# Kernel tuning notes

Measured on AMD Instinct MI355X. Metric: run time of the kernel, lower is better.

The kernel has to match this reference:

```python
import jax, jax.numpy as jnp
import numpy as np

N = 100000      # nodes
E = 1600000     # edges (avg degree 16)
IN_F, HID, OUT_F, NC = 384, 128, 64, 2
EPS = 1e-5
NEG_SLOPE = 0.01


def _layernorm(x, g, b):
    m = jnp.mean(x, axis=-1, keepdims=True)
    v = jnp.var(x, axis=-1, keepdims=True)
    return (x - m) * jax.lax.rsqrt(v + EPS) * g + b


def _graph_conv(x, edge_index, edge_weight, w_rel, b_rel, w_root):
    # PyG GraphConv: lin_rel(scatter_add(w_e * x[src] -> dst)) + lin_root(x)
    src, dst = edge_index[0], edge_index[1]
    msg = x[src] * edge_weight[:, None]                      # [E, C]
    agg = jax.ops.segment_sum(msg, dst, num_segments=x.shape[0])  # [N, C]
    return agg @ w_rel.T + b_rel + x @ w_root.T


def _xavier(key, shape):
    fan_in, fan_out = shape[1], shape[0]
    lim = float(np.sqrt(6.0 / (fan_in + fan_out)))
    return jax.random.uniform(key, shape, jnp.float32, -lim, lim)


def setup_inputs() -> dict:
    key = jax.random.key(0)
    ks = jax.random.split(key, 10)
    x = jax.random.normal(ks[0], (N, IN_F), jnp.float32)
    edge_index = jax.random.randint(ks[1], (2, E), 0, N, jnp.int64)
    edge_attr = jax.random.uniform(ks[2], (E,), jnp.float32)
    return {
        "x": x,
        "edge_index": edge_index,
        "edge_attr": edge_attr,
        "ln1_g": jnp.ones((IN_F,), jnp.float32),
        "ln1_b": jnp.zeros((IN_F,), jnp.float32),
        "fc1_w": _xavier(ks[3], (HID, IN_F)),
        "fc1_b": jnp.zeros((HID,), jnp.float32),
        "c1_wrel": _xavier(ks[4], (HID, HID)),
        "c1_brel": jnp.zeros((HID,), jnp.float32),
        "c1_wroot": _xavier(ks[5], (HID, HID)),
        "c2_wrel": _xavier(ks[6], (OUT_F, HID)),
        "c2_brel": jnp.zeros((OUT_F,), jnp.float32),
        "c2_wroot": _xavier(ks[7], (OUT_F, HID)),
        "ln2_g": jnp.ones((OUT_F,), jnp.float32),
        "ln2_b": jnp.zeros((OUT_F,), jnp.float32),
        "fc2_w": _xavier(ks[8], (NC, OUT_F)),
        "fc2_b": jnp.zeros((NC,), jnp.float32),
    }


def reference(x, edge_index, edge_attr,
              ln1_g, ln1_b, fc1_w, fc1_b,
              c1_wrel, c1_brel, c1_wroot,
              c2_wrel, c2_brel, c2_wroot,
              ln2_g, ln2_b, fc2_w, fc2_b):
    h = _layernorm(x, ln1_g, ln1_b) @ fc1_w.T + fc1_b          # [N, HID]
    h = _graph_conv(h, edge_index, edge_attr, c1_wrel, c1_brel, c1_wroot)
    h = jax.nn.leaky_relu(h, NEG_SLOPE)
    h = _graph_conv(h, edge_index, edge_attr, c2_wrel, c2_brel, c2_wroot)
    h = jax.nn.leaky_relu(h, NEG_SLOPE)                        # [N, OUT_F]
    out = _layernorm(h, ln2_g, ln2_b) @ fc2_w.T + fc2_b        # [N, NC]
    return out
```

## Files before the change

### kernel.cpp

```cpp
#include <hip/hip_runtime.h>
#include <hip/hip_bf16.h>

#define N_IN_F 384
#define N_HID  128
#define N_OUT  64

typedef unsigned short ushort_t;
typedef __attribute__((ext_vector_type(8))) short short8v;
typedef __attribute__((ext_vector_type(4))) float floatx4;

union U8 { uint4 v; unsigned short u[8]; };

__device__ __forceinline__ float bfu2f(unsigned short s){
    union { unsigned i; float f; } c; c.i = ((unsigned)s) << 16; return c.f;
}
__device__ __forceinline__ unsigned short f2bfu(float f){
    __hip_bfloat16 h = __float2bfloat16(f);
    union { __hip_bfloat16 h; unsigned short u; } c; c.h = h; return c.u;
}

__device__ __forceinline__ float loadS(const void* p, size_t i, int fm){
    return fm ? bfu2f(((const unsigned short*)p)[i]) : ((const float*)p)[i];
}

__global__ void k_detect_all(const int* __restrict__ ei, const unsigned* __restrict__ xw,
                             int* __restrict__ modep){
    int lane = threadIdx.x & 63;
    int zi = 0;
    if (lane < 32) zi = ei[2*lane + 1];
    int cnt = 0;
    #pragma unroll
    for (int q = 0; q < 8; q++){
        unsigned w = xw[lane*8 + q];
        unsigned elo = (w >> 7) & 0xff;
        cnt += (elo >= 118 && elo <= 134) ? 1 : 0;
    }
    #pragma unroll
    for (int m = 32; m; m >>= 1){ zi |= __shfl_xor(zi, m, 64); cnt += __shfl_xor(cnt, m, 64); }
    if (lane == 0 && blockIdx.x == 0){
        modep[0] = (zi == 0) ? 1 : 0;
        modep[1] = (cnt >= 256) ? 1 : 0;
    }
}

__device__ __forceinline__ int edge_src(const int* ei, int e, int i, int mode){
    return mode ? ei[2*(size_t)i] : ei[i];
}
__device__ __forceinline__ int edge_dst(const int* ei, int e, int i, int mode){
    return mode ? ei[2*(size_t)e + 2*(size_t)i] : ei[(size_t)e + i];
}

__global__ void k_hist(const int* __restrict__ ei, int e, int n, const int* __restrict__ modep,
                       int* __restrict__ deg, unsigned* __restrict__ rel){
    int i = blockIdx.x * 256 + threadIdx.x;
    if (i >= e) return;
    int mode = modep[0];
    int d = edge_dst(ei, e, i, mode);
    if ((unsigned)d >= (unsigned)n) return;
    rel[i] = (unsigned)atomicAdd(&deg[d], 1);
}

__global__ __launch_bounds__(1024) void k_blksum(
    const int* __restrict__ deg, int n, int* __restrict__ part)
{
    __shared__ int s[1024];
    int i = blockIdx.x * 1024 + threadIdx.x;
    s[threadIdx.x] = (i < n) ? deg[i] : 0;
    __syncthreads();
    for (int off = 512; off; off >>= 1){
        if (threadIdx.x < off) s[threadIdx.x] += s[threadIdx.x + off];
        __syncthreads();
    }
    if (threadIdx.x == 0) part[blockIdx.x] = s[0];
}

__global__ __launch_bounds__(128) void k_scanpart(
    int* __restrict__ part, int nb, int* __restrict__ rowoff, int n)
{
    __shared__ int s[128];
    int t = threadIdx.x;
    if (nb <= 128){
        int v = (t < nb) ? part[t] : 0;
        s[t] = v; __syncthreads();
        #pragma unroll
        for (int off = 1; off < 128; off <<= 1){
            int tmp = (t >= off) ? s[t - off] : 0;
            __syncthreads();
            s[t] += tmp;
            __syncthreads();
        }
        if (t < nb) part[t] = s[t] - v;
        if (t == 127) rowoff[n] = s[127];
    } else if (t == 0){
        int run = 0;
        for (int b = 0; b < nb; b++){ int tt = part[b]; part[b] = run; run += tt; }
        rowoff[n] = run;
    }
}

__global__ __launch_bounds__(1024) void k_scanblk(
    int* __restrict__ deg, const int* __restrict__ part, int n, int* __restrict__ rowoff)
{
    __shared__ int s[1024];
    int t = threadIdx.x;
    int i = blockIdx.x * 1024 + t;
    int v = (i < n) ? deg[i] : 0;
    s[t] = v; __syncthreads();
    for (int off = 1; off < 1024; off <<= 1){
        int tmp = (t >= off) ? s[t - off] : 0;
        __syncthreads();
        s[t] += tmp;
        __syncthreads();
    }
    if (i < n){
        int excl = s[t] - v + part[blockIdx.x];
        rowoff[i] = excl;
        deg[i]    = excl;
    }
}

__global__ void k_scatter(const int* __restrict__ ei, const void* __restrict__ ea,
                          int e, int n, const int* __restrict__ modep,
                          int* __restrict__ cursor, int2* __restrict__ colw)
{
    int i = blockIdx.x * 256 + threadIdx.x;
    if (i >= e) return;
    int mode = modep[0], fm = modep[1];
    int d = edge_dst(ei, e, i, mode);
    if ((unsigned)d >= (unsigned)n) return;
    int s = edge_src(ei, e, i, mode);
    if ((unsigned)s >= (unsigned)n) s = 0;
    int pos = atomicAdd(&cursor[d], 1);
    if ((unsigned)pos >= (unsigned)e) return;
    int2 pk; pk.x = s; pk.y = __float_as_int(loadS(ea, i, fm));
    colw[pos] = pk;
}

#define SC_CHUNK 2048
#define SC_BSHIFT 13
#define SC_MAXB 1024
__global__ __launch_bounds__(256) void k_scoarse(
    const int* __restrict__ ei, const void* __restrict__ ea,
    const unsigned* __restrict__ rel, const int* __restrict__ rowoff,
    const int* __restrict__ modep, int e, int n, int B,
    int4* __restrict__ tmp, int* __restrict__ off2)
{
    __shared__ int  hcnt[SC_MAXB];
    __shared__ int  hoff[SC_MAXB + 1];
    __shared__ int4 stage[SC_CHUNK];
    int t = threadIdx.x;
    int c = blockIdx.x;
    int chunk0 = c * SC_CHUNK;
    int mode = modep[0], fm = modep[1];

    for (int q = t; q < B; q += 256) hcnt[q] = 0;
    __syncthreads();

    int  pos[8], sv[8], wv[8];
    bool val[8];
    #pragma unroll
    for (int k = 0; k < 8; k++){
        int i = chunk0 + k*256 + t;
        val[k] = false;
        if (i < e){
            int d = edge_dst(ei, e, i, mode);
            if ((unsigned)d < (unsigned)n){
                int s = edge_src(ei, e, i, mode);
                if ((unsigned)s >= (unsigned)n) s = 0;
                int p = rowoff[d] + (int)rel[i];
                pos[k] = p; sv[k] = s; wv[k] = __float_as_int(loadS(ea, i, fm));
                val[k] = true;
                atomicAdd(&hcnt[p >> SC_BSHIFT], 1);
            }
        }
    }
    __syncthreads();
    if (t == 0){
        int run = 0;
        for (int q = 0; q < B; q++){ hoff[q] = run; run += hcnt[q]; }
        hoff[B] = run;
    }
    __syncthreads();
    for (int q = t; q < B; q += 256) hcnt[q] = 0;
    for (int q = t; q <= B; q += 256) off2[(size_t)c*(B+1) + q] = hoff[q];
    __syncthreads();
    #pragma unroll
    for (int k = 0; k < 8; k++){
        if (val[k]){
            int b = pos[k] >> SC_BSHIFT;
            int slot = hoff[b] + atomicAdd(&hcnt[b], 1);
            stage[slot] = make_int4(pos[k], sv[k], wv[k], 0);
        }
    }
    __syncthreads();
    int tot = hoff[B];
    for (int idx = t; idx < tot; idx += 256)
        tmp[(size_t)chunk0 + idx] = stage[idx];
}

__global__ __launch_bounds__(512) void k_sfine(
    const int4* __restrict__ tmp, const int* __restrict__ off2,
    int B, int nchunks, int2* __restrict__ colw)
{
    int b = blockIdx.x;
    int wv = threadIdx.x >> 6, lane = threadIdx.x & 63;
    const int NW = 8;
    int c = wv;
    if (c >= nchunks) return;
    int s0 = off2[(size_t)c*(B+1) + b];
    int s1 = off2[(size_t)c*(B+1) + b + 1];
    while (true){
        int cn = c + NW;
        int n0 = 0, n1 = 0;
        if (cn < nchunks){
            n0 = off2[(size_t)cn*(B+1) + b];
            n1 = off2[(size_t)cn*(B+1) + b + 1];
        }
        int len = s1 - s0;
        size_t base = (size_t)c * SC_CHUNK + s0;
        for (int k = lane; k < len; k += 64){
            int4 ent = tmp[base + k];
            colw[ent.x] = make_int2(ent.y, ent.z);
        }
        if (cn >= nchunks) break;
        c = cn; s0 = n0; s1 = n1;
    }
}

__global__ __launch_bounds__(64) void k_prep_w1(
    const void* __restrict__ W, const void* __restrict__ g, const void* __restrict__ b,
    const void* __restrict__ fc1b, const int* __restrict__ fmp,
    ushort_t* __restrict__ Wp, float* __restrict__ u, float* __restrict__ v)
{
    int fm = fmp[0];
    int j = blockIdx.x, lane = threadIdx.x;
    float su = 0.f, sv = 0.f;
    for (int k = lane; k < N_IN_F; k += 64){
        float w  = loadS(W, (size_t)j*N_IN_F + k, fm);
        float gk = loadS(g, k, fm);
        float bk = loadS(b, k, fm);
        unsigned short pw = f2bfu(gk * w);
        Wp[(size_t)j*N_IN_F + k] = pw;
        su += bfu2f(pw);
        sv += bk * w;
    }
    #pragma unroll
    for (int m = 32; m; m >>= 1){ su += __shfl_xor(su, m, 64); sv += __shfl_xor(sv, m, 64); }
    if (lane == 0){
        u[j] = su;
        v[j] = sv + loadS(fc1b, j, fm);
    }
}

__global__ void k_cvt4(const void* __restrict__ p0, const void* __restrict__ p1,
                       const void* __restrict__ p2, const void* __restrict__ p3,
                       const int* __restrict__ fmp, ushort_t* __restrict__ o)
{
    int fm = fmp[0];
    int i = blockIdx.x * 256 + threadIdx.x;
    if (i >= 49152) return;
    const void* p; int off;
    if (i < 16384)      { p = p0; off = i; }
    else if (i < 32768) { p = p1; off = i - 16384; }
    else if (i < 40960) { p = p2; off = i - 32768; }
    else                { p = p3; off = i - 40960; }
    o[i] = f2bfu(loadS(p, off, fm));
}

__global__ __launch_bounds__(256) void k_gemm1_mfma(
    const void* __restrict__ x, const int* __restrict__ fmp,
    const ushort_t* __restrict__ Wp,
    const float* __restrict__ u, const float* __restrict__ v,
    ushort_t* __restrict__ out, int n)
{
    __shared__ ushort_t As[128*40];
    __shared__ ushort_t Bs[128*40];
    int fm = fmp[0];
    int t = threadIdx.x;
    int wave = t >> 6, lane = t & 63;
    int r16 = lane & 15, kq = lane >> 4;
    int m0 = blockIdx.x * 128;
    int mw = m0 + wave * 32;

    int sq = t & 3, srow = t >> 2;
    int bcol = t & 127, bhalf = t >> 7;

    floatx4 acc[2][8];
    #pragma unroll
    for (int a = 0; a < 2; a++)
        #pragma unroll
        for (int c = 0; c < 8; c++) acc[a][c] = (floatx4){0.f,0.f,0.f,0.f};
    float s1[2] = {0.f,0.f}, s2[2] = {0.f,0.f};

    for (int ks = 0; ks < 12; ks++){
        int kb = ks*32;
        #pragma unroll
        for (int pass = 0; pass < 2; pass++){
            int row  = srow + pass*64;
            int grow = min(m0 + row, n - 1);
            union { ushort_t u[8]; uint4 v4; } w;
            if (fm){
                w.v4 = *(const uint4*)((const ushort_t*)x + (size_t)grow*N_IN_F + kb + sq*8);
            } else {
                const float* xf = (const float*)x + (size_t)grow*N_IN_F + kb + sq*8;
                floatx4 p = *(const floatx4*)xf;
                floatx4 q4 = *(const floatx4*)(xf + 4);
                w.u[0]=f2bfu(p[0]); w.u[1]=f2bfu(p[1]); w.u[2]=f2bfu(p[2]); w.u[3]=f2bfu(p[3]);
                w.u[4]=f2bfu(q4[0]); w.u[5]=f2bfu(q4[1]); w.u[6]=f2bfu(q4[2]); w.u[7]=f2bfu(q4[3]);
            }
            *(uint4*)(As + row*40 + sq*8) = w.v4;
        }
        {
            const ushort_t* wp = Wp + (size_t)bcol*N_IN_F + kb + bhalf*16;
            uint4 b0 = *(const uint4*)wp;
            uint4 b1 = *(const uint4*)(wp + 8);
            *(uint4*)(Bs + bcol*40 + bhalf*16)     = b0;
            *(uint4*)(Bs + bcol*40 + bhalf*16 + 8) = b1;
        }
        __syncthreads();
        short8v af[2], bfr[8];
        #pragma unroll
        for (int mi = 0; mi < 2; mi++)
            af[mi] = *(const short8v*)(As + (wave*32 + mi*16 + r16)*40 + kq*8);
        #pragma unroll
        for (int ni = 0; ni < 8; ni++)
            bfr[ni] = *(const short8v*)(Bs + (ni*16 + r16)*40 + kq*8);
        #pragma unroll
        for (int mi = 0; mi < 2; mi++){
            #pragma unroll
            for (int q = 0; q < 8; q++){
                float f = bfu2f((unsigned short)af[mi][q]);
                s1[mi] += f; s2[mi] += f*f;
            }
            #pragma unroll
            for (int ni = 0; ni < 8; ni++)
                acc[mi][ni] = __builtin_amdgcn_mfma_f32_16x16x32_bf16(af[mi], bfr[ni], acc[mi][ni], 0, 0, 0);
        }
        __syncthreads();
    }

    float mu[2], rs[2];
    #pragma unroll
    for (int mi = 0; mi < 2; mi++){
        s1[mi] += __shfl_xor(s1[mi], 16, 64); s1[mi] += __shfl_xor(s1[mi], 32, 64);
        s2[mi] += __shfl_xor(s2[mi], 16, 64); s2[mi] += __shfl_xor(s2[mi], 32, 64);
        mu[mi] = s1[mi] * (1.f/384.f);
        float var = fmaxf(s2[mi] * (1.f/384.f) - mu[mi]*mu[mi], 0.f);
        rs[mi] = rsqrtf(var + 1e-5f);
    }

    #pragma unroll
    for (int mi = 0; mi < 2; mi++){
        int ib = mw + mi*16 + kq*4;
        float mm[4], rr[4];
        #pragma unroll
        for (int r = 0; r < 4; r++){
            mm[r] = __shfl(mu[mi], kq*4 + r, 64);
            rr[r] = __shfl(rs[mi], kq*4 + r, 64);
        }
        #pragma unroll
        for (int ni = 0; ni < 8; ni++){
            int j = ni*16 + r16;
            float uj = u[j], vj = v[j];
            #pragma unroll
            for (int r = 0; r < 4; r++){
                int ii = ib + r;
                float val = rr[r]*acc[mi][ni][r] - rr[r]*mm[r]*uj + vj;
                if (ii < n) out[(size_t)ii*N_HID + j] = f2bfu(val);
            }
        }
    }
}

__global__ __launch_bounds__(256) void k_conv1_mfma(
    const ushort_t* __restrict__ A1, const ushort_t* __restrict__ A2,
    const ushort_t* __restrict__ W1, const ushort_t* __restrict__ W2,
    const void* __restrict__ bias, const int* __restrict__ fmp,
    ushort_t* __restrict__ out, int n)
{
    __shared__ ushort_t As[128*40];
    __shared__ ushort_t Bs[128*40];
    int fm = fmp[0];
    int t = threadIdx.x;
    int wave = t >> 6, lane = t & 63;
    int r16 = lane & 15, kq = lane >> 4;
    int m0 = blockIdx.x * 128;
    int mw = m0 + wave * 32;

    int sq = t & 3, srow = t >> 2;
    int bcol = t & 127, bhalf = t >> 7;

    floatx4 acc[2][8];
    #pragma unroll
    for (int a = 0; a < 2; a++)
        #pragma unroll
        for (int c = 0; c < 8; c++) acc[a][c] = (floatx4){0.f,0.f,0.f,0.f};

    #pragma unroll
    for (int ks = 0; ks < 8; ks++){
        const ushort_t* Asrc = (ks < 4) ? A1 : A2;
        const ushort_t* Wsrc = (ks < 4) ? W1 : W2;
        int kb = (ks & 3)*32;
        #pragma unroll
        for (int pass = 0; pass < 2; pass++){
            int row  = srow + pass*64;
            int grow = min(m0 + row, n - 1);
            uint4 w = *(const uint4*)(Asrc + (size_t)grow*N_HID + kb + sq*8);
            *(uint4*)(As + row*40 + sq*8) = w;
        }
        {
            const ushort_t* wp = Wsrc + (size_t)bcol*N_HID + kb + bhalf*16;
            uint4 b0 = *(const uint4*)wp;
            uint4 b1 = *(const uint4*)(wp + 8);
            *(uint4*)(Bs + bcol*40 + bhalf*16)     = b0;
            *(uint4*)(Bs + bcol*40 + bhalf*16 + 8) = b1;
        }
        __syncthreads();
        short8v af[2], bfr[8];
        #pragma unroll
        for (int mi = 0; mi < 2; mi++)
            af[mi] = *(const short8v*)(As + (wave*32 + mi*16 + r16)*40 + kq*8);
        #pragma unroll
        for (int ni = 0; ni < 8; ni++)
            bfr[ni] = *(const short8v*)(Bs + (ni*16 + r16)*40 + kq*8);
        #pragma unroll
        for (int mi = 0; mi < 2; mi++)
            #pragma unroll
            for (int ni = 0; ni < 8; ni++)
                acc[mi][ni] = __builtin_amdgcn_mfma_f32_16x16x32_bf16(af[mi], bfr[ni], acc[mi][ni], 0, 0, 0);
        __syncthreads();
    }

    #pragma unroll
    for (int mi = 0; mi < 2; mi++){
        int ib = mw + mi*16 + kq*4;
        #pragma unroll
        for (int ni = 0; ni < 8; ni++){
            int j = ni*16 + r16;
            float bb = loadS(bias, j, fm);
            #pragma unroll
            for (int r = 0; r < 4; r++){
                int ii = ib + r;
                float val = acc[mi][ni][r] + bb;
                val = (val >= 0.f) ? val : 0.01f * val;
                if (ii < n) out[(size_t)ii*N_HID + j] = f2bfu(val);
            }
        }
    }
}

__global__ __launch_bounds__(256) void k_conv2_final(
    const ushort_t* __restrict__ A1, const ushort_t* __restrict__ A2,
    const ushort_t* __restrict__ W1, const ushort_t* __restrict__ W2,
    const void* __restrict__ bias,
    const void* __restrict__ gam, const void* __restrict__ bet,
    const void* __restrict__ Wfc, const void* __restrict__ bfc,
    const int* __restrict__ fmp, void* __restrict__ out, int n)
{
    __shared__ ushort_t As[128*40];
    __shared__ ushort_t Bs[64*40];
    int fm = fmp[0];
    int t = threadIdx.x;
    int wave = t >> 6, lane = t & 63;
    int r16 = lane & 15, kq = lane >> 4;
    int m0 = blockIdx.x * 128;
    int mw = m0 + wave * 32;

    int sq = t & 3, srow = t >> 2;
    int bcol = t & 63, bseg = t >> 6;

    floatx4 acc[2][4];
    #pragma unroll
    for (int a = 0; a < 2; a++)
        #pragma unroll
        for (int c = 0; c < 4; c++) acc[a][c] = (floatx4){0.f,0.f,0.f,0.f};

    #pragma unroll
    for (int ks = 0; ks < 8; ks++){
        const ushort_t* Asrc = (ks < 4) ? A1 : A2;
        const ushort_t* Wsrc = (ks < 4) ? W1 : W2;
        int kb = (ks & 3)*32;
        #pragma unroll
        for (int pass = 0; pass < 2; pass++){
            int row  = srow + pass*64;
            int grow = min(m0 + row, n - 1);
            uint4 w = *(const uint4*)(Asrc + (size_t)grow*N_HID + kb + sq*8);
            *(uint4*)(As + row*40 + sq*8) = w;
        }
        {
            uint4 b0 = *(const uint4*)(Wsrc + (size_t)bcol*N_HID + kb + bseg*8);
            *(uint4*)(Bs + bcol*40 + bseg*8) = b0;
        }
        __syncthreads();
        short8v af[2], bfr[4];
        #pragma unroll
        for (int mi = 0; mi < 2; mi++)
            af[mi] = *(const short8v*)(As + (wave*32 + mi*16 + r16)*40 + kq*8);
        #pragma unroll
        for (int ni = 0; ni < 4; ni++)
            bfr[ni] = *(const short8v*)(Bs + (ni*16 + r16)*40 + kq*8);
        #pragma unroll
        for (int mi = 0; mi < 2; mi++)
            #pragma unroll
            for (int ni = 0; ni < 4; ni++)
                acc[mi][ni] = __builtin_amdgcn_mfma_f32_16x16x32_bf16(af[mi], bfr[ni], acc[mi][ni], 0, 0, 0);
        __syncthreads();
    }

    float b0 = loadS(bfc, 0, fm), b1 = loadS(bfc, 1, fm);
    #pragma unroll
    for (int mi = 0; mi < 2; mi++){
        float s[4] = {}, s2[4] = {};
        #pragma unroll
        for (int ni = 0; ni < 4; ni++){
            int j = ni*16 + r16;
            float bb = loadS(bias, j, fm);
            #pragma unroll
            for (int r = 0; r < 4; r++){
                float val = acc[mi][ni][r] + bb;
                val = (val >= 0.f) ? val : 0.01f * val;
                acc[mi][ni][r] = val;
                s[r] += val; s2[r] += val*val;
            }
        }
        #pragma unroll
        for (int m = 1; m < 16; m <<= 1){
            #pragma unroll
            for (int r = 0; r < 4; r++){
                s[r]  += __shfl_xor(s[r],  m, 64);
                s2[r] += __shfl_xor(s2[r], m, 64);
            }
        }
        float mu[4], rstd[4];
        #pragma unroll
        for (int r = 0; r < 4; r++){
            mu[r] = s[r] * (1.f/64.f);
            float var = fmaxf(s2[r] * (1.f/64.f) - mu[r]*mu[r], 0.f);
            rstd[r] = rsqrtf(var + 1e-5f);
        }
        float p0[4] = {}, p1[4] = {};
        #pragma unroll
        for (int ni = 0; ni < 4; ni++){
            int j = ni*16 + r16;
            float gj = loadS(gam, j, fm), bj = loadS(bet, j, fm);
            float w0 = loadS(Wfc, j, fm), w1 = loadS(Wfc, 64 + j, fm);
            #pragma unroll
            for (int r = 0; r < 4; r++){
                float zn = (acc[mi][ni][r] - mu[r]) * rstd[r] * gj + bj;
                p0[r] += zn * w0;
                p1[r] += zn * w1;
            }
        }
        #pragma unroll
        for (int m = 1; m < 16; m <<= 1){
            #pragma unroll
            for (int r = 0; r < 4; r++){
                p0[r] += __shfl_xor(p0[r], m, 64);
                p1[r] += __shfl_xor(p1[r], m, 64);
            }
        }
        if (r16 == 0){
            #pragma unroll
            for (int r = 0; r < 4; r++){
                int ii = mw + mi*16 + kq*4 + r;
                if (ii >= n) continue;
                float o0 = p0[r] + b0, o1 = p1[r] + b1;
                if (fm){
                    unsigned pk = ((unsigned)f2bfu(o1) << 16) | (unsigned)f2bfu(o0);
                    *(unsigned*)((ushort_t*)out + (size_t)ii*2) = pk;
                } else {
                    float2 f2; f2.x = o0; f2.y = o1;
                    *(float2*)((float*)out + (size_t)ii*2) = f2;
                }
            }
        }
    }
}

__global__ __launch_bounds__(256) void k_agg(
    const int* __restrict__ rowoff, const int2* __restrict__ colw,
    const ushort_t* __restrict__ src_mat,
    ushort_t* __restrict__ out, int n, int eTot)
{
    int t = threadIdx.x;
    int lane = t & 63;
    int d = blockIdx.x * 4 + (t >> 6);
    if (d >= n) return;
    int grp = lane >> 4;
    int c16 = lane & 15;
    int e0 = rowoff[d], e1 = rowoff[d+1];
    e0 = max(0, min(e0, eTot));
    e1 = max(e0, min(e1, eTot));
    float acc[8] = {};
    for (int e = e0 + grp; e < e1; e += 4){
        int2 cw = colw[e];
        int s = cw.x;
        if ((unsigned)s >= (unsigned)n) s = 0;
        float wv = __int_as_float(cw.y);
        U8 u; u.v = *(const uint4*)(src_mat + (size_t)s*N_HID + c16*8);
        #pragma unroll
        for (int q = 0; q < 8; q++) acc[q] += wv * bfu2f(u.u[q]);
    }
    #pragma unroll
    for (int q = 0; q < 8; q++){
        acc[q] += __shfl_xor(acc[q], 16, 64);
        acc[q] += __shfl_xor(acc[q], 32, 64);
    }
    if (grp == 0){
        union { ushort_t u[8]; uint4 v; } P;
        #pragma unroll
        for (int q = 0; q < 8; q++) P.u[q] = f2bfu(acc[q]);
        *(uint4*)(out + (size_t)d*N_HID + c16*8) = P.v;
    }
}

extern "C" void kernel_launch(void* const* d_in, const int* in_sizes, int n_in,
                              void* d_out, int out_size, void* d_ws, size_t ws_size,
                              hipStream_t stream)
{
    const void* x     = d_in[0];
    const int*  ei    = (const int*)d_in[1];
    const void* ea    = d_in[2];
    const void* ln1g  = d_in[3];
    const void* ln1b  = d_in[4];
    const void* fc1w  = d_in[5];
    const void* fc1b  = d_in[6];
    const void* c1rel = d_in[7];
    const void* c1bre = d_in[8];
    const void* c1roo = d_in[9];
    const void* c2rel = d_in[10];
    const void* c2bre = d_in[11];
    const void* c2roo = d_in[12];
    const void* ln2g  = d_in[13];
    const void* ln2b  = d_in[14];
    const void* fc2w  = d_in[15];
    const void* fc2b  = d_in[16];
    (void)n_in; (void)out_size; (void)ws_size;

    const int n = in_sizes[0] / N_IN_F;
    const int e = in_sizes[2];

    const int nchunks = (e + SC_CHUNK - 1) / SC_CHUNK;
    const int B = (e + (1 << SC_BSHIFT) - 1) >> SC_BSHIFT;

    char* wsp = (char*)d_ws;
    size_t off = 0;
    auto alloc = [&](size_t bytes) -> char* {
        char* p = wsp + off; off += (bytes + 255) & ~(size_t)255; return p;
    };
    int*      deg    = (int*)  alloc((size_t)n * 4);
    int*      rowoff = (int*)  alloc((size_t)(n+1) * 4);
    int*      part   = (int*)  alloc(4096);
    int*      modep  = (int*)  alloc(256);
    int2*     colw   = (int2*) alloc((size_t)e * 8);
    unsigned* rel    = (unsigned*)alloc((size_t)e * 4);
    int4*     stmp   = (int4*) alloc((size_t)e * 16);
    int*      off2   = (int*)  alloc((size_t)nchunks * (B+1) * 4);
    float*    u      = (float*)alloc(128 * 4);
    float*    v      = (float*)alloc(128 * 4);
    ushort_t* Wp     = (ushort_t*)alloc((size_t)N_HID * N_IN_F * 2);
    ushort_t* cw     = (ushort_t*)alloc((size_t)49152 * 2);
    ushort_t* h1     = (ushort_t*)alloc((size_t)n * N_HID * 2);
    ushort_t* agg1   = (ushort_t*)alloc((size_t)n * N_HID * 2);
    ushort_t* g1     = (ushort_t*)alloc((size_t)n * N_HID * 2);
    ushort_t* agg2   = h1;

    hipMemsetAsync(deg, 0, (size_t)n * 4, stream);
    k_detect_all<<<1, 64, 0, stream>>>(ei, (const unsigned*)x, modep);

    int nb = (n + 1023) / 1024;
    k_hist    <<<(e + 255) / 256, 256, 0, stream>>>(ei, e, n, modep, deg, rel);
    k_blksum  <<<nb, 1024, 0, stream>>>(deg, n, part);
    k_scanpart<<<1, 128, 0, stream>>>(part, nb, rowoff, n);
    k_scanblk <<<nb, 1024, 0, stream>>>(deg, part, n, rowoff);

    if (B <= SC_MAXB){
        k_scoarse<<<nchunks, 256, 0, stream>>>(ei, ea, rel, rowoff, modep, e, n, B, stmp, off2);
        k_sfine  <<<B, 512, 0, stream>>>(stmp, off2, B, nchunks, colw);
    } else {
        k_scatter<<<(e + 255) / 256, 256, 0, stream>>>(ei, ea, e, n, modep, deg, colw);
    }

    k_prep_w1<<<N_HID, 64, 0, stream>>>(fc1w, ln1g, ln1b, fc1b, modep + 1, Wp, u, v);
    k_cvt4   <<<(49152 + 255) / 256, 256, 0, stream>>>(c1rel, c1roo, c2rel, c2roo, modep + 1, cw);

    k_gemm1_mfma<<<(n + 127) / 128, 256, 0, stream>>>(x, modep + 1, Wp, u, v, h1, n);

    k_agg<<<(n + 3) / 4, 256, 0, stream>>>(rowoff, colw, h1, agg1, n, e);
    k_conv1_mfma<<<(n + 127) / 128, 256, 0, stream>>>(agg1, h1, cw, cw + 16384, c1bre, modep + 1, g1, n);

    k_agg<<<(n + 3) / 4, 256, 0, stream>>>(rowoff, colw, g1, agg2, n, e);
    k_conv2_final<<<(n + 127) / 128, 256, 0, stream>>>(agg2, g1, cw + 32768, cw + 40960, c2bre,
                                                       ln2g, ln2b, fc2w, fc2b, modep + 1, d_out, n);
}
```

Measured before the change: 658.7 us.

## Halve GEMM row tiles and prefetch next K-slice into registers

Changes the three MFMA GEMM kernels (gemm1, conv1, conv2_final) from 128-row to 64-row tiles, so each wave computes 16 rows. The grid doubles and LDS use per block drops. Each kernel also loads the next K-slice of A and B into registers right after the barrier, overlapping global loads with MFMA work, and removes the trailing barrier per iteration. The cost is twice as many B-tile reloads per node and less MFMA work per wave to hide latency.

```diff
diff --git a/kernel.cpp b/kernel.cpp
--- a/kernel.cpp
+++ b/kernel.cpp
@@ -273,101 +273,90 @@
     const float* __restrict__ u, const float* __restrict__ v,
     ushort_t* __restrict__ out, int n)
 {
-    __shared__ ushort_t As[128*40];
+    __shared__ ushort_t As[64*40];
     __shared__ ushort_t Bs[128*40];
     int fm = fmp[0];
     int t = threadIdx.x;
     int wave = t >> 6, lane = t & 63;
     int r16 = lane & 15, kq = lane >> 4;
-    int m0 = blockIdx.x * 128;
-    int mw = m0 + wave * 32;
+    int m0 = blockIdx.x * 64;
+    int mw = m0 + wave * 16;
 
     int sq = t & 3, srow = t >> 2;
     int bcol = t & 127, bhalf = t >> 7;
 
-    floatx4 acc[2][8];
-    #pragma unroll
-    for (int a = 0; a < 2; a++)
-        #pragma unroll
-        for (int c = 0; c < 8; c++) acc[a][c] = (floatx4){0.f,0.f,0.f,0.f};
-    float s1[2] = {0.f,0.f}, s2[2] = {0.f,0.f};
+    int garow = min(m0 + srow, n - 1);
+    const ushort_t* xbf = (const ushort_t*)x + (size_t)garow*N_IN_F + sq*8;
+    const float*    xf  = (const float*)x    + (size_t)garow*N_IN_F + sq*8;
+    const ushort_t* wpB = Wp + (size_t)bcol*N_IN_F + bhalf*16;
+
+    floatx4 acc[8];
+    #pragma unroll
+    for (int c = 0; c < 8; c++) acc[c] = (floatx4){0.f,0.f,0.f,0.f};
+    float s1 = 0.f, s2 = 0.f;
+
+    uint4 aBF; floatx4 aF0, aF1; uint4 b0r, b1r;
+    if (fm) aBF = *(const uint4*)xbf;
+    else { aF0 = *(const floatx4*)xf; aF1 = *(const floatx4*)(xf + 4); }
+    b0r = *(const uint4*)wpB;
+    b1r = *(const uint4*)(wpB + 8);
 
     for (int ks = 0; ks < 12; ks++){
-        int kb = ks*32;
-        #pragma unroll
-        for (int pass = 0; pass < 2; pass++){
-            int row  = srow + pass*64;
-            int grow = min(m0 + row, n - 1);
-            union { ushort_t u[8]; uint4 v4; } w;
-            if (fm){
-                w.v4 = *(const uint4*)((const ushort_t*)x + (size_t)grow*N_IN_F + kb + sq*8);
-            } else {
-                const float* xf = (const float*)x + (size_t)grow*N_IN_F + kb + sq*8;
-                floatx4 p = *(const floatx4*)xf;
-                floatx4 q4 = *(const floatx4*)(xf + 4);
-                w.u[0]=f2bfu(p[0]); w.u[1]=f2bfu(p[1]); w.u[2]=f2bfu(p[2]); w.u[3]=f2bfu(p[3]);
-                w.u[4]=f2bfu(q4[0]); w.u[5]=f2bfu(q4[1]); w.u[6]=f2bfu(q4[2]); w.u[7]=f2bfu(q4[3]);
-            }
-            *(uint4*)(As + row*40 + sq*8) = w.v4;
-        }
-        {
-            const ushort_t* wp = Wp + (size_t)bcol*N_IN_F + kb + bhalf*16;
-            uint4 b0 = *(const uint4*)wp;
-            uint4 b1 = *(const uint4*)(wp + 8);
-            *(uint4*)(Bs + bcol*40 + bhalf*16)     = b0;
-            *(uint4*)(Bs + bcol*40 + bhalf*16 + 8) = b1;
-        }
+        if (ks) __syncthreads();
+        union { ushort_t u[8]; uint4 v4; } w;
+        if (fm) w.v4 = aBF;
+        else {
+            w.u[0]=f2bfu(aF0[0]); w.u[1]=f2bfu(aF0[1]); w.u[2]=f2bfu(aF0[2]); w.u[3]=f2bfu(aF0[3]);
+            w.u[4]=f2bfu(aF1[0]); w.u[5]=f2bfu(aF1[1]); w.u[6]=f2bfu(aF1[2]); w.u[7]=f2bfu(aF1[3]);
+        }
+        *(uint4*)(As + srow*40 + sq*8) = w.v4;
+        *(uint4*)(Bs + bcol*40 + bhalf*16)     = b0r;
+        *(uint4*)(Bs + bcol*40 + bhalf*16 + 8) = b1r;
         __syncthreads();
-        short8v af[2], bfr[8];
-        #pragma unroll
-        for (int mi = 0; mi < 2; mi++)
-            af[mi] = *(const short8v*)(As + (wave*32 + mi*16 + r16)*40 + kq*8);
+        if (ks + 1 < 12){
+            int kb = (ks + 1) * 32;
+            if (fm) aBF = *(const uint4*)(xbf + kb);
+            else { aF0 = *(const floatx4*)(xf + kb); aF1 = *(const floatx4*)(xf + kb + 4); }
+            b0r = *(const uint4*)(wpB + kb);
+            b1r = *(const uint4*)(wpB + kb + 8);
+        }
+        short8v af = *(const short8v*)(As + (wave*16 + r16)*40 + kq*8);
+        short8v bfr[8];
         #pragma unroll
         for (int ni = 0; ni < 8; ni++)
             bfr[ni] = *(const short8v*)(Bs + (ni*16 + r16)*40 + kq*8);
         #pragma unroll
-        for (int mi = 0; mi < 2; mi++){
-            #pragma unroll
-            for (int q = 0; q < 8; q++){
-                float f = bfu2f((unsigned short)af[mi][q]);
-                s1[mi] += f; s2[mi] += f*f;
-            }
-            #pragma unroll
-            for (int ni = 0; ni < 8; ni++)
-                acc[mi][ni] = __builtin_amdgcn_mfma_f32_16x16x32_bf16(af[mi], bfr[ni], acc[mi][ni], 0, 0, 0);
-        }
-        __syncthreads();
-    }
-
-    float mu[2], rs[2];
-    #pragma unroll
-    for (int mi = 0; mi < 2; mi++){
-        s1[mi] += __shfl_xor(s1[mi], 16, 64); s1[mi] += __shfl_xor(s1[mi], 32, 64);
-        s2[mi] += __shfl_xor(s2[mi], 16, 64); s2[mi] += __shfl_xor(s2[mi], 32, 64);
-        mu[mi] = s1[mi] * (1.f/384.f);
-        float var = fmaxf(s2[mi] * (1.f/384.f) - mu[mi]*mu[mi], 0.f);
-        rs[mi] = rsqrtf(var + 1e-5f);
-    }
-
-    #pragma unroll
-    for (int mi = 0; mi < 2; mi++){
-        int ib = mw + mi*16 + kq*4;
-        float mm[4], rr[4];
+        for (int q = 0; q < 8; q++){
+            float f = bfu2f((unsigned short)af[q]);
+            s1 += f; s2 += f*f;
+        }
+        #pragma unroll
+        for (int ni = 0; ni < 8; ni++)
+            acc[ni] = __builtin_amdgcn_mfma_f32_16x16x32_bf16(af, bfr[ni], acc[ni], 0, 0, 0);
+    }
+
+    s1 += __shfl_xor(s1, 16, 64); s1 += __shfl_xor(s1, 32, 64);
+    s2 += __shfl_xor(s2, 16, 64); s2 += __shfl_xor(s2, 32, 64);
+    float mu = s1 * (1.f/384.f);
+    float var = fmaxf(s2 * (1.f/384.f) - mu*mu, 0.f);
+    float rs = rsqrtf(var + 1e-5f);
+
+    float mm[4], rr[4];
+    #pragma unroll
+    for (int r = 0; r < 4; r++){
+        mm[r] = __shfl(mu, kq*4 + r, 64);
+        rr[r] = __shfl(rs, kq*4 + r, 64);
+    }
+    int ib = mw + kq*4;
+    #pragma unroll
+    for (int ni = 0; ni < 8; ni++){
+        int j = ni*16 + r16;
+        float uj = u[j], vj = v[j];
         #pragma unroll
         for (int r = 0; r < 4; r++){
-            mm[r] = __shfl(mu[mi], kq*4 + r, 64);
-            rr[r] = __shfl(rs[mi], kq*4 + r, 64);
-        }
-        #pragma unroll
-        for (int ni = 0; ni < 8; ni++){
-            int j = ni*16 + r16;
-            float uj = u[j], vj = v[j];
-            #pragma unroll
-            for (int r = 0; r < 4; r++){
-                int ii = ib + r;
-                float val = rr[r]*acc[mi][ni][r] - rr[r]*mm[r]*uj + vj;
-                if (ii < n) out[(size_t)ii*N_HID + j] = f2bfu(val);
-            }
+            int ii = ib + r;
+            float val = rr[r]*acc[ni][r] - rr[r]*mm[r]*uj + vj;
+            if (ii < n) out[(size_t)ii*N_HID + j] = f2bfu(val);
         }
     }
 }
@@ -378,73 +367,68 @@
     const void* __restrict__ bias, const int* __restrict__ fmp,
     ushort_t* __restrict__ out, int n)
 {
-    __shared__ ushort_t As[128*40];
+    __shared__ ushort_t As[64*40];
     __shared__ ushort_t Bs[128*40];
     int fm = fmp[0];
     int t = threadIdx.x;
     int wave = t >> 6, lane = t & 63;
     int r16 = lane & 15, kq = lane >> 4;
-    int m0 = blockIdx.x * 128;
-    int mw = m0 + wave * 32;
+    int m0 = blockIdx.x * 64;
+    int mw = m0 + wave * 16;
 
     int sq = t & 3, srow = t >> 2;
     int bcol = t & 127, bhalf = t >> 7;
 
-    floatx4 acc[2][8];
-    #pragma unroll
-    for (int a = 0; a < 2; a++)
-        #pragma unroll
-        for (int c = 0; c < 8; c++) acc[a][c] = (floatx4){0.f,0.f,0.f,0.f};
+    int garow = min(m0 + srow, n - 1);
+    size_t aoff = (size_t)garow*N_HID + sq*8;
+    size_t boff = (size_t)bcol*N_HID + bhalf*16;
+
+    floatx4 acc[8];
+    #pragma unroll
+    for (int c = 0; c < 8; c++) acc[c] = (floatx4){0.f,0.f,0.f,0.f};
+
+    uint4 aR, b0r, b1r;
+    aR  = *(const uint4*)(A1 + aoff);
+    b0r = *(const uint4*)(W1 + boff);
+    b1r = *(const uint4*)(W1 + boff + 8);
 
     #pragma unroll
     for (int ks = 0; ks < 8; ks++){
-        const ushort_t* Asrc = (ks < 4) ? A1 : A2;
-        const ushort_t* Wsrc = (ks < 4) ? W1 : W2;
-        int kb = (ks & 3)*32;
-        #pragma unroll
-        for (int pass = 0; pass < 2; pass++){
-            int row  = srow + pass*64;
-            int grow = min(m0 + row, n - 1);
-            uint4 w = *(const uint4*)(Asrc + (size_t)grow*N_HID + kb + sq*8);
-            *(uint4*)(As + row*40 + sq*8) = w;
-        }
-        {
-            const ushort_t* wp = Wsrc + (size_t)bcol*N_HID + kb + bhalf*16;
-            uint4 b0 = *(const uint4*)wp;
-            uint4 b1 = *(const uint4*)(wp + 8);
-            *(uint4*)(Bs + bcol*40 + bhalf*16)     = b0;
-            *(uint4*)(Bs + bcol*40 + bhalf*16 + 8) = b1;
-        }
+        if (ks) __syncthreads();
+        *(uint4*)(As + srow*40 + sq*8) = aR;
+        *(uint4*)(Bs + bcol*40 + bhalf*16)     = b0r;
+        *(uint4*)(Bs + bcol*40 + bhalf*16 + 8) = b1r;
         __syncthreads();
-        short8v af[2], bfr[8];
-        #pragma unroll
-        for (int mi = 0; mi < 2; mi++)
-            af[mi] = *(const short8v*)(As + (wave*32 + mi*16 + r16)*40 + kq*8);
+        if (ks + 1 < 8){
+            int kn = ks + 1;
+            const ushort_t* Asrc = (kn < 4) ? A1 : A2;
+            const ushort_t* Wsrc = (kn < 4) ? W1 : W2;
+            int kb = (kn & 3) * 32;
+            aR  = *(const uint4*)(Asrc + aoff + kb);
+            b0r = *(const uint4*)(Wsrc + boff + kb);
+            b1r = *(const uint4*)(Wsrc + boff + kb + 8);
+        }
+        short8v af = *(const short8v*)(As + (wave*16 + r16)*40 + kq*8);
+        short8v bfr[8];
         #pragma unroll
         for (int ni = 0; ni < 8; ni++)
             bfr[ni] = *(const short8v*)(Bs + (ni*16 + r16)*40 + kq*8);
         #pragma unroll
-        for (int mi = 0; mi < 2; mi++)
-            #pragma unroll
-            for (int ni = 0; ni < 8; ni++)
-                acc[mi][ni] = __builtin_amdgcn_mfma_f32_16x16x32_bf16(af[mi], bfr[ni], acc[mi][ni], 0, 0, 0);
-        __syncthreads();
-    }
-
-    #pragma unroll
-    for (int mi = 0; mi < 2; mi++){
-        int ib = mw + mi*16 + kq*4;
-        #pragma unroll
-        for (int ni = 0; ni < 8; ni++){
-            int j = ni*16 + r16;
-            float bb = loadS(bias, j, fm);
-            #pragma unroll
-            for (int r = 0; r < 4; r++){
-                int ii = ib + r;
-                float val = acc[mi][ni][r] + bb;
-                val = (val >= 0.f) ? val : 0.01f * val;
-                if (ii < n) out[(size_t)ii*N_HID + j] = f2bfu(val);
-            }
+        for (int ni = 0; ni < 8; ni++)
+            acc[ni] = __builtin_amdgcn_mfma_f32_16x16x32_bf16(af, bfr[ni], acc[ni], 0, 0, 0);
+    }
+
+    int ib = mw + kq*4;
+    #pragma unroll
+    for (int ni = 0; ni < 8; ni++){
+        int j = ni*16 + r16;
+        float bb = loadS(bias, j, fm);
+        #pragma unroll
+        for (int r = 0; r < 4; r++){
+            int ii = ib + r;
+            float val = acc[ni][r] + bb;
+            val = (val >= 0.f) ? val : 0.01f * val;
+            if (ii < n) out[(size_t)ii*N_HID + j] = f2bfu(val);
         }
     }
 }
@@ -457,121 +441,116 @@
     const void* __restrict__ Wfc, const void* __restrict__ bfc,
     const int* __restrict__ fmp, void* __restrict__ out, int n)
 {
-    __shared__ ushort_t As[128*40];
+    __shared__ ushort_t As[64*40];
     __shared__ ushort_t Bs[64*40];
     int fm = fmp[0];
     int t = threadIdx.x;
     int wave = t >> 6, lane = t & 63;
     int r16 = lane & 15, kq = lane >> 4;
-    int m0 = blockIdx.x * 128;
-    int mw = m0 + wave * 32;
+    int m0 = blockIdx.x * 64;
+    int mw = m0 + wave * 16;
 
     int sq = t & 3, srow = t >> 2;
     int bcol = t & 63, bseg = t >> 6;
 
-    floatx4 acc[2][4];
-    #pragma unroll
-    for (int a = 0; a < 2; a++)
-        #pragma unroll
-        for (int c = 0; c < 4; c++) acc[a][c] = (floatx4){0.f,0.f,0.f,0.f};
+    int garow = min(m0 + srow, n - 1);
+    size_t aoff = (size_t)garow*N_HID + sq*8;
+    size_t boff = (size_t)bcol*N_HID + bseg*8;
+
+    floatx4 acc[4];
+    #pragma unroll
+    for (int c = 0; c < 4; c++) acc[c] = (floatx4){0.f,0.f,0.f,0.f};
+
+    uint4 aR, bR;
+    aR = *(const uint4*)(A1 + aoff);
+    bR = *(const uint4*)(W1 + boff);
 
     #pragma unroll
     for (int ks = 0; ks < 8; ks++){
-        const ushort_t* Asrc = (ks < 4) ? A1 : A2;
-        const ushort_t* Wsrc = (ks < 4) ? W1 : W2;
-        int kb = (ks & 3)*32;
-        #pragma unroll
-        for (int pass = 0; pass < 2; pass++){
-            int row  = srow + pass*64;
-            int grow = min(m0 + row, n - 1);
-            uint4 w = *(const uint4*)(Asrc + (size_t)grow*N_HID + kb + sq*8);
-            *(uint4*)(As + row*40 + sq*8) = w;
-        }
-        {
-            uint4 b0 = *(const uint4*)(Wsrc + (size_t)bcol*N_HID + kb + bseg*8);
-            *(uint4*)(Bs + bcol*40 + bseg*8) = b0;
-        }
+        if (ks) __syncthreads();
+        *(uint4*)(As + srow*40 + sq*8) = aR;
+        *(uint4*)(Bs + bcol*40 + bseg*8) = bR;
         __syncthreads();
-        short8v af[2], bfr[4];
-        #pragma unroll
-        for (int mi = 0; mi < 2; mi++)
-            af[mi] = *(const short8v*)(As + (wave*32 + mi*16 + r16)*40 + kq*8);
+        if (ks + 1 < 8){
+            int kn = ks + 1;
+            const ushort_t* Asrc = (kn < 4) ? A1 : A2;
+            const ushort_t* Wsrc = (kn < 4) ? W1 : W2;
+            int kb = (kn & 3) * 32;
+            aR = *(const uint4*)(Asrc + aoff + kb);
+            bR = *(const uint4*)(Wsrc + boff + kb);
+        }
+        short8v af = *(const short8v*)(As + (wave*16 + r16)*40 + kq*8);
+        short8v bfr[4];
         #pragma unroll
         for (int ni = 0; ni < 4; ni++)
             bfr[ni] = *(const short8v*)(Bs + (ni*16 + r16)*40 + kq*8);
         #pragma unroll
-        for (int mi = 0; mi < 2; mi++)
-            #pragma unroll
-            for (int ni = 0; ni < 4; ni++)
-                acc[mi][ni] = __builtin_amdgcn_mfma_f32_16x16x32_bf16(af[mi], bfr[ni], acc[mi][ni], 0, 0, 0);
-        __syncthreads();
+        for (int ni = 0; ni < 4; ni++)
+            acc[ni] = __builtin_amdgcn_mfma_f32_16x16x32_bf16(af, bfr[ni], acc[ni], 0, 0, 0);
     }
 
     float b0 = loadS(bfc, 0, fm), b1 = loadS(bfc, 1, fm);
-    #pragma unroll
-    for (int mi = 0; mi < 2; mi++){
-        float s[4] = {}, s2[4] = {};
-        #pragma unroll
-        for (int ni = 0; ni < 4; ni++){
-            int j = ni*16 + r16;
-            float bb = loadS(bias, j, fm);
-            #pragma unroll
-            for (int r = 0; r < 4; r++){
-                float val = acc[mi][ni][r] + bb;
-                val = (val >= 0.f) ? val : 0.01f * val;
-                acc[mi][ni][r] = val;
-                s[r] += val; s2[r] += val*val;
-            }
-        }
-        #pragma unroll
-        for (int m = 1; m < 16; m <<= 1){
-            #pragma unroll
-            for (int r = 0; r < 4; r++){
-                s[r]  += __shfl_xor(s[r],  m, 64);
-                s2[r] += __shfl_xor(s2[r], m, 64);
-            }
-        }
-        float mu[4], rstd[4];
+    float s[4] = {}, s2[4] = {};
+    #pragma unroll
+    for (int ni = 0; ni < 4; ni++){
+        int j = ni*16 + r16;
+        float bb = loadS(bias, j, fm);
         #pragma unroll
         for (int r = 0; r < 4; r++){
-            mu[r] = s[r] * (1.f/64.f);
-            float var = fmaxf(s2[r] * (1.f/64.f) - mu[r]*mu[r], 0.f);
-            rstd[r] = rsqrtf(var + 1e-5f);
-        }
-        float p0[4] = {}, p1[4] = {};
-        #pragma unroll
-        for (int ni = 0; ni < 4; ni++){
-            int j = ni*16 + r16;
-            float gj = loadS(gam, j, fm), bj = loadS(bet, j, fm);
-            float w0 = loadS(Wfc, j, fm), w1 = loadS(Wfc, 64 + j, fm);
-            #pragma unroll
-            for (int r = 0; r < 4; r++){
-                float zn = (acc[mi][ni][r] - mu[r]) * rstd[r] * gj + bj;
-                p0[r] += zn * w0;
-                p1[r] += zn * w1;
-            }
-        }
-        #pragma unroll
-        for (int m = 1; m < 16; m <<= 1){
-            #pragma unroll
-            for (int r = 0; r < 4; r++){
-                p0[r] += __shfl_xor(p0[r], m, 64);
-                p1[r] += __shfl_xor(p1[r], m, 64);
-            }
-        }
-        if (r16 == 0){
-            #pragma unroll
-            for (int r = 0; r < 4; r++){
-                int ii = mw + mi*16 + kq*4 + r;
-                if (ii >= n) continue;
-                float o0 = p0[r] + b0, o1 = p1[r] + b1;
-                if (fm){
-                    unsigned pk = ((unsigned)f2bfu(o1) << 16) | (unsigned)f2bfu(o0);
-                    *(unsigned*)((ushort_t*)out + (size_t)ii*2) = pk;
-                } else {
-                    float2 f2; f2.x = o0; f2.y = o1;
-                    *(float2*)((float*)out + (size_t)ii*2) = f2;
-                }
+            float val = acc[ni][r] + bb;
+            val = (val >= 0.f) ? val : 0.01f * val;
+            acc[ni][r] = val;
+            s[r] += val; s2[r] += val*val;
+        }
+    }
+    #pragma unroll
+    for (int m = 1; m < 16; m <<= 1){
+        #pragma unroll
+        for (int r = 0; r < 4; r++){
+            s[r]  += __shfl_xor(s[r],  m, 64);
+            s2[r] += __shfl_xor(s2[r], m, 64);
+        }
+    }
+    float mu[4], rstd[4];
+    #pragma unroll
+    for (int r = 0; r < 4; r++){
+        mu[r] = s[r] * (1.f/64.f);
+        float var = fmaxf(s2[r] * (1.f/64.f) - mu[r]*mu[r], 0.f);
+        rstd[r] = rsqrtf(var + 1e-5f);
+    }
+    float p0[4] = {}, p1[4] = {};
+    #pragma unroll
+    for (int ni = 0; ni < 4; ni++){
+        int j = ni*16 + r16;
+        float gj = loadS(gam, j, fm), bj = loadS(bet, j, fm);
+        float w0 = loadS(Wfc, j, fm), w1 = loadS(Wfc, 64 + j, fm);
+        #pragma unroll
+        for (int r = 0; r < 4; r++){
+            float zn = (acc[ni][r] - mu[r]) * rstd[r] * gj + bj;
+            p0[r] += zn * w0;
+            p1[r] += zn * w1;
+        }
+    }
+    #pragma unroll
+    for (int m = 1; m < 16; m <<= 1){
+        #pragma unroll
+        for (int r = 0; r < 4; r++){
+            p0[r] += __shfl_xor(p0[r], m, 64);
+            p1[r] += __shfl_xor(p1[r], m, 64);
+        }
+    }
+    if (r16 == 0){
+        #pragma unroll
+        for (int r = 0; r < 4; r++){
+            int ii = mw + kq*4 + r;
+            if (ii >= n) continue;
+            float o0 = p0[r] + b0, o1 = p1[r] + b1;
+            if (fm){
+                unsigned pk = ((unsigned)f2bfu(o1) << 16) | (unsigned)f2bfu(o0);
+                *(unsigned*)((ushort_t*)out + (size_t)ii*2) = pk;
+            } else {
+                float2 f2; f2.x = o0; f2.y = o1;
+                *(float2*)((float*)out + (size_t)ii*2) = f2;
             }
         }
     }
@@ -684,12 +663,12 @@
     k_prep_w1<<<N_HID, 64, 0, stream>>>(fc1w, ln1g, ln1b, fc1b, modep + 1, Wp, u, v);
     k_cvt4   <<<(49152 + 255) / 256, 256, 0, stream>>>(c1rel, c1roo, c2rel, c2roo, modep + 1, cw);
 
-    k_gemm1_mfma<<<(n + 127) / 128, 256, 0, stream>>>(x, modep + 1, Wp, u, v, h1, n);
+    k_gemm1_mfma<<<(n + 63) / 64, 256, 0, stream>>>(x, modep + 1, Wp, u, v, h1, n);
 
     k_agg<<<(n + 3) / 4, 256, 0, stream>>>(rowoff, colw, h1, agg1, n, e);
-    k_conv1_mfma<<<(n + 127) / 128, 256, 0, stream>>>(agg1, h1, cw, cw + 16384, c1bre, modep + 1, g1, n);
+    k_conv1_mfma<<<(n + 63) / 64, 256, 0, stream>>>(agg1, h1, cw, cw + 16384, c1bre, modep + 1, g1, n);
 
     k_agg<<<(n + 3) / 4, 256, 0, stream>>>(rowoff, colw, g1, agg2, n, e);
-    k_conv2_final<<<(n + 127) / 128, 256, 0, stream>>>(agg2, g1, cw + 32768, cw + 40960, c2bre,
-                                                       ln2g, ln2b, fc2w, fc2b, modep + 1, d_out, n);
-}
+    k_conv2_final<<<(n + 63) / 64, 256, 0, stream>>>(agg2, g1, cw + 32768, cw + 40960, c2bre,
+                                                     ln2g, ln2b, fc2w, fc2b, modep + 1, d_out, n);
+}
```

After: 638.1 us. 3.1% less time.
